# Performance work log

Measured on AMD Instinct MI355X. Metric: run time of the kernel, lower is better.

Reference implementation:

```python
import jax, jax.numpy as jnp
import numpy as np

N_A = 50000
N_B = 50000
E = 500000
D = 128


def setup_inputs() -> dict:
    key = jax.random.key(0)
    ks = jax.random.split(key, 16)
    s = 0.02
    inp = {
        "x_a": jax.random.normal(ks[0], (N_A, D), jnp.float32),
        "x_b": jax.random.normal(ks[1], (N_B, D), jnp.float32),
        # shared GraphEdgeWeight params
        "Wp": jax.random.normal(ks[2], (D, D), jnp.float32) * s,
        "bp": jnp.zeros((D,), jnp.float32),
        "Wc": jax.random.normal(ks[3], (D, D), jnp.float32) * s,
        "bc": jnp.zeros((D,), jnp.float32),
        "W1": jax.random.normal(ks[4], (D, 3 * D), jnp.float32) * s,
        "b1": jnp.zeros((D,), jnp.float32),
        "W2": jax.random.normal(ks[5], (1, D), jnp.float32) * s,
        "b2": jnp.zeros((1,), jnp.float32),
        # GraphConv params for edge type A->B
        "Wrel_ab": jax.random.normal(ks[6], (D, D), jnp.float32) * s,
        "brel_ab": jnp.zeros((D,), jnp.float32),
        "Wroot_ab": jax.random.normal(ks[7], (D, D), jnp.float32) * s,
        "broot_ab": jnp.zeros((D,), jnp.float32),
        # GraphConv params for edge type B->A
        "Wrel_ba": jax.random.normal(ks[8], (D, D), jnp.float32) * s,
        "brel_ba": jnp.zeros((D,), jnp.float32),
        "Wroot_ba": jax.random.normal(ks[9], (D, D), jnp.float32) * s,
        "broot_ba": jnp.zeros((D,), jnp.float32),
        # edge indices: row0 = src node ids, row1 = dst node ids
        "ei_ab": jax.random.randint(ks[10], (2, E), 0, N_A),
        "ei_ba": jax.random.randint(ks[11], (2, E), 0, N_B),
    }
    return inp


def _edge_type_conv(x_src, x_dst, ei, Wp, bp, Wc, bc, W1, b1, W2, b2,
                    Wrel, brel, Wroot, broot, n_dst):
    # gather endpoint features per edge  [E, D]
    par = x_src[ei[0]]
    cld = x_dst[ei[1]]
    # GraphEdgeWeight: encoders (Linear + LeakyReLU; dropout inactive in eval)
    ep = jax.nn.leaky_relu(par @ Wp.T + bp, negative_slope=0.01)
    ec = jax.nn.leaky_relu(cld @ Wc.T + bc, negative_slope=0.01)
    feat = jnp.concatenate([ep, ec, jnp.abs(par - cld)], axis=-1)  # [E, 3D]
    h = jax.nn.relu(feat @ W1.T + b1)                              # [E, D]
    w = jax.nn.sigmoid(h @ W2.T + b2)[:, 0]                        # [E]
    # GraphConv: out_i = Wrel @ sum_{j->i} w_e x_j + Wroot @ x_i (+ biases)
    msg = jax.ops.segment_sum(par * w[:, None], ei[1], num_segments=n_dst)
    return msg @ Wrel.T + brel + x_dst @ Wroot.T + broot


def reference(x_a, x_b, Wp, bp, Wc, bc, W1, b1, W2, b2,
              Wrel_ab, brel_ab, Wroot_ab, broot_ab,
              Wrel_ba, brel_ba, Wroot_ba, broot_ba,
              ei_ab, ei_ba):
    out_b = _edge_type_conv(x_a, x_b, ei_ab, Wp, bp, Wc, bc, W1, b1, W2, b2,
                            Wrel_ab, brel_ab, Wroot_ab, broot_ab, N_B)
    out_a = _edge_type_conv(x_b, x_a, ei_ba, Wp, bp, Wc, bc, W1, b1, W2, b2,
                            Wrel_ba, brel_ba, Wroot_ba, broot_ba, N_A)
    return out_a, out_b
```

## Files before the change

kernel.cpp:

```cpp
#include <hip/hip_runtime.h>
#include <hip/hip_bf16.h>

typedef unsigned short u16;
typedef __attribute__((ext_vector_type(8))) short bf16x8;
typedef __attribute__((ext_vector_type(2))) short s16x2;
typedef __attribute__((ext_vector_type(4))) float f32x4;

#define N_NODES 50000
#define EDGES 500000
#define WPT 31250
#define NWAVES 3125
#define NBLK 782

__device__ __forceinline__ u16 f2bf(float f) {
  return __builtin_bit_cast(u16, __float2bfloat16(f));
}
__device__ __forceinline__ float bf2f(u16 u) {
  return __builtin_bit_cast(float, ((unsigned)u) << 16);
}
__device__ __forceinline__ float bfe(bf16x8 v, int j) {
  return bf2f((u16)v[j]);
}

__device__ __forceinline__ void pk_atomic_bf16(u16* addr, float lo, float hi) {
#if __has_builtin(__builtin_amdgcn_global_atomic_fadd_v2bf16)
  s16x2 v;
  v[0] = (short)f2bf(lo);
  v[1] = (short)f2bf(hi);
  __builtin_amdgcn_global_atomic_fadd_v2bf16(
      (__attribute__((address_space(1))) s16x2*)addr, v);
#else
  unsigned* p = (unsigned*)addr;
  unsigned old = *p, assumed;
  do {
    assumed = old;
    float l2 = bf2f((u16)(assumed & 0xffff)) + lo;
    float h2 = bf2f((u16)(assumed >> 16)) + hi;
    unsigned nv = (unsigned)f2bf(l2) | ((unsigned)f2bf(h2) << 16);
    old = atomicCAS(p, assumed, nv);
  } while (old != assumed);
#endif
}

__global__ __launch_bounds__(256) void prep_weights(
    const float* __restrict__ Wp, const float* __restrict__ Wc,
    const float* __restrict__ W1,
    const float* __restrict__ Wrel_ab, const float* __restrict__ Wroot_ab,
    const float* __restrict__ Wrel_ba, const float* __restrict__ Wroot_ba,
    u16* __restrict__ out)
{
  int tid = blockIdx.x * 256 + threadIdx.x;
  int m = tid >> 14;
  int idx = tid & 16383;
  int r = idx >> 7;
  int c = idx & 127;
  float val;
  switch (m) {
    case 0: val = Wp[r * 128 + c]; break;
    case 1: val = Wc[r * 128 + c]; break;
    case 2: val = W1[r * 384 + c]; break;
    case 3: val = W1[r * 384 + 128 + c]; break;
    case 4: val = W1[r * 384 + 256 + c]; break;
    case 5: val = Wrel_ab[r * 128 + c]; break;
    case 6: val = Wroot_ab[r * 128 + c]; break;
    case 7: val = Wrel_ba[r * 128 + c]; break;
    default: val = Wroot_ba[r * 128 + c]; break;
  }
  out[tid] = f2bf(val);
}

__global__ __launch_bounds__(256) void cast_x(
    const float* __restrict__ xa, const float* __restrict__ xb,
    u16* __restrict__ oa, u16* __restrict__ ob)
{
  int t = blockIdx.x * 256 + threadIdx.x;
  const int HALF = (N_NODES * 128) / 8;
  const float* src;
  u16* dst;
  int idx;
  if (t < HALF) { src = xa; dst = oa; idx = t * 8; }
  else          { src = xb; dst = ob; idx = (t - HALF) * 8; }
  f32x4 a = *(const f32x4*)(src + idx);
  f32x4 b = *(const f32x4*)(src + idx + 4);
  bf16x8 o;
#pragma unroll
  for (int j = 0; j < 4; j++) {
    o[j]     = (short)f2bf(a[j]);
    o[j + 4] = (short)f2bf(b[j]);
  }
  *(bf16x8*)(dst + idx) = o;
}

__global__ __launch_bounds__(256) void encoder2(
    const u16* __restrict__ xa_bf, const u16* __restrict__ xb_bf,
    const u16* __restrict__ Wp_b, const float* __restrict__ bp,
    const u16* __restrict__ Wc_b, const float* __restrict__ bc,
    const u16* __restrict__ W1a_b, const float* __restrict__ b1,
    const u16* __restrict__ W1b_b,
    u16* __restrict__ u_a, u16* __restrict__ v_a,
    u16* __restrict__ u_b, u16* __restrict__ v_b)
{
  __shared__ u16 tile[4][2176];
  int widx = threadIdx.x >> 6;
  int w = blockIdx.x * 4 + widx;
  int type = (w >= NBLK * 4) ? 1 : 0;
  int nw = w - type * NBLK * 4;
  if (nw >= NWAVES) nw = NWAVES - 1;
  const u16* xbf = type ? xb_bf : xa_bf;
  u16* u_out = type ? u_b : u_a;
  u16* v_out = type ? v_b : v_a;
  int row0 = nw * 16;
  int lane = threadIdx.x & 63;
  int col = lane & 15;
  int quad = lane >> 4;
  u16* tl = tile[widx];

  bf16x8 af[4];
#pragma unroll
  for (int ks = 0; ks < 4; ks++)
    af[ks] = *(const bf16x8*)(xbf + (size_t)(row0 + col) * 128 + ks * 32 + quad * 8);

  f32x4 zero = {0.f, 0.f, 0.f, 0.f};

  for (int chain = 0; chain < 2; chain++) {
    const u16* Wenc = chain ? Wc_b : Wp_b;
    const float* benc = chain ? bc : bp;
    const u16* Wmix = chain ? W1b_b : W1a_b;
    const float* bmix = chain ? nullptr : b1;
    u16* outp = chain ? v_out : u_out;

    f32x4 acc[8];
#pragma unroll
    for (int nt = 0; nt < 8; nt++) acc[nt] = zero;
#pragma unroll
    for (int ks = 0; ks < 4; ks++) {
      const u16* wp = Wenc + col * 128 + ks * 32 + quad * 8;
#pragma unroll
      for (int nt = 0; nt < 8; nt++) {
        bf16x8 bf = *(const bf16x8*)(wp + nt * 2048);
        acc[nt] = __builtin_amdgcn_mfma_f32_16x16x32_bf16(af[ks], bf, acc[nt], 0, 0, 0);
      }
    }
#pragma unroll
    for (int nt = 0; nt < 8; nt++) {
      float be = benc[nt * 16 + col];
#pragma unroll
      for (int r = 0; r < 4; r++) {
        float v = acc[nt][r] + be;
        v = v > 0.f ? v : 0.01f * v;
        tl[(quad * 4 + r) * 136 + nt * 16 + col] = f2bf(v);
      }
    }
    bf16x8 a2[4];
#pragma unroll
    for (int ks = 0; ks < 4; ks++)
      a2[ks] = *(const bf16x8*)&tl[col * 136 + ks * 32 + quad * 8];

    f32x4 acc2[8];
#pragma unroll
    for (int nt = 0; nt < 8; nt++) acc2[nt] = zero;
#pragma unroll
    for (int ks = 0; ks < 4; ks++) {
      const u16* wp = Wmix + col * 128 + ks * 32 + quad * 8;
#pragma unroll
      for (int nt = 0; nt < 8; nt++) {
        bf16x8 bf = *(const bf16x8*)(wp + nt * 2048);
        acc2[nt] = __builtin_amdgcn_mfma_f32_16x16x32_bf16(a2[ks], bf, acc2[nt], 0, 0, 0);
      }
    }
#pragma unroll
    for (int nt = 0; nt < 8; nt++) {
      float bm = bmix ? bmix[nt * 16 + col] : 0.f;
#pragma unroll
      for (int r = 0; r < 4; r++)
        outp[(size_t)(row0 + quad * 4 + r) * 128 + nt * 16 + col] = f2bf(acc2[nt][r] + bm);
    }
  }
}

__global__ __launch_bounds__(256) void out_gemm2(
    const u16* __restrict__ xa_bf, const u16* __restrict__ xb_bf,
    const u16* __restrict__ msgX_a, const u16* __restrict__ msgX_b,
    const u16* __restrict__ Wrelba_b, const u16* __restrict__ Wrelab_b,
    const u16* __restrict__ Wrootba_b, const u16* __restrict__ Wrootab_b,
    const float* __restrict__ brel_ba, const float* __restrict__ broot_ba,
    const float* __restrict__ brel_ab, const float* __restrict__ broot_ab,
    float* __restrict__ out_a, float* __restrict__ out_b)
{
  int w = blockIdx.x * 4 + (threadIdx.x >> 6);
  int type = (w >= NBLK * 4) ? 1 : 0;
  int nw = w - type * NBLK * 4;
  if (nw >= NWAVES) return;
  const u16* xbf = type ? xb_bf : xa_bf;
  const u16* msg = type ? msgX_b : msgX_a;
  const u16* Wrel = type ? Wrelab_b : Wrelba_b;
  const u16* Wroot = type ? Wrootab_b : Wrootba_b;
  const float* brel = type ? brel_ab : brel_ba;
  const float* broot = type ? broot_ab : broot_ba;
  float* outp = type ? out_b : out_a;
  int row0 = nw * 16;
  int lane = threadIdx.x & 63;
  int col = lane & 15;
  int quad = lane >> 4;

  bf16x8 ax[4], am[4];
#pragma unroll
  for (int ks = 0; ks < 4; ks++) {
    ax[ks] = *(const bf16x8*)(xbf + (size_t)(row0 + col) * 128 + ks * 32 + quad * 8);
    am[ks] = *(const bf16x8*)(msg + (size_t)(row0 + col) * 128 + ks * 32 + quad * 8);
  }

  f32x4 zero = {0.f, 0.f, 0.f, 0.f};
  f32x4 acc[8];
#pragma unroll
  for (int nt = 0; nt < 8; nt++) acc[nt] = zero;
#pragma unroll
  for (int ks = 0; ks < 4; ks++) {
    const u16* wp1 = Wrel + col * 128 + ks * 32 + quad * 8;
    const u16* wp2 = Wroot + col * 128 + ks * 32 + quad * 8;
#pragma unroll
    for (int nt = 0; nt < 8; nt++) {
      bf16x8 b1f = *(const bf16x8*)(wp1 + nt * 2048);
      acc[nt] = __builtin_amdgcn_mfma_f32_16x16x32_bf16(am[ks], b1f, acc[nt], 0, 0, 0);
      bf16x8 b2f = *(const bf16x8*)(wp2 + nt * 2048);
      acc[nt] = __builtin_amdgcn_mfma_f32_16x16x32_bf16(ax[ks], b2f, acc[nt], 0, 0, 0);
    }
  }
#pragma unroll
  for (int nt = 0; nt < 8; nt++) {
    int c = nt * 16 + col;
    float b = brel[c] + broot[c];
#pragma unroll
    for (int r = 0; r < 4; r++)
      outp[(size_t)(row0 + quad * 4 + r) * 128 + c] = acc[nt][r] + b;
  }
}

__global__ __launch_bounds__(256) void edge_fused(
    const u16* __restrict__ xa_bf, const u16* __restrict__ xb_bf,
    const int* __restrict__ ei_ab, const int* __restrict__ ei_ba,
    const u16* __restrict__ W1c,
    const u16* __restrict__ u_a, const u16* __restrict__ v_a,
    const u16* __restrict__ u_b, const u16* __restrict__ v_b,
    const float* __restrict__ W2, const float* __restrict__ b2p,
    u16* __restrict__ msgX_a, u16* __restrict__ msgX_b)
{
  __shared__ u16 tld[4][2176];
  int widx = threadIdx.x >> 6;
  int w = blockIdx.x * 4 + widx;
  int type = (w >= WPT) ? 1 : 0;
  int e0 = (w - type * WPT) * 16;
  const u16* xs = type ? xb_bf : xa_bf;
  const u16* xd = type ? xa_bf : xb_bf;
  const int* ei = type ? ei_ba : ei_ab;
  const u16* uT = type ? u_b : u_a;
  const u16* vT = type ? v_a : v_b;
  u16* msgX     = type ? msgX_a : msgX_b;

  int lane = threadIdx.x & 63;
  int col = lane & 15;
  int quad = lane >> 4;

  int em = e0 + col;
  int si = ei[em];
  int di = ei[EDGES + em];

  bf16x8 af[4];
  bf16x8 df[4];
#pragma unroll
  for (int ks = 0; ks < 4; ks++) {
    af[ks] = *(const bf16x8*)(xs + (size_t)si * 128 + ks * 32 + quad * 8);
    bf16x8 d8 = *(const bf16x8*)(xd + (size_t)di * 128 + ks * 32 + quad * 8);
#pragma unroll
    for (int j = 0; j < 8; j++)
      df[ks][j] = (short)f2bf(__builtin_fabsf(bfe(af[ks], j) - bfe(d8, j)));
  }

  f32x4 zero = {0.f, 0.f, 0.f, 0.f};
  f32x4 acc[8];
#pragma unroll
  for (int nt = 0; nt < 8; nt++) acc[nt] = zero;
#pragma unroll
  for (int ks = 0; ks < 4; ks++) {
    const u16* wp = W1c + col * 128 + ks * 32 + quad * 8;
#pragma unroll
    for (int nt = 0; nt < 8; nt++) {
      bf16x8 bf = *(const bf16x8*)(wp + nt * 2048);
      acc[nt] = __builtin_amdgcn_mfma_f32_16x16x32_bf16(df[ks], bf, acc[nt], 0, 0, 0);
    }
  }

  u16* tl = tld[widx];
#pragma unroll
  for (int nt = 0; nt < 8; nt++)
#pragma unroll
    for (int r = 0; r < 4; r++)
      tl[(quad * 4 + r) * 136 + nt * 16 + col] = f2bf(acc[nt][r]);

  int e = e0 + (lane >> 2);
  int s2 = ei[e];
  int d2 = ei[EDGES + e];
  int c0 = (lane & 3) * 32;
  const u16* trow = &tl[(lane >> 2) * 136 + c0];
  const u16* urow = uT + (size_t)s2 * 128 + c0;
  const u16* vrow = vT + (size_t)d2 * 128 + c0;

  float p = 0.f;
#pragma unroll
  for (int k = 0; k < 4; k++) {
    bf16x8 tt = *(const bf16x8*)(trow + k * 8);
    bf16x8 uu = *(const bf16x8*)(urow + k * 8);
    bf16x8 vv = *(const bf16x8*)(vrow + k * 8);
    f32x4 w0 = *(const f32x4*)(W2 + c0 + k * 8);
    f32x4 w1 = *(const f32x4*)(W2 + c0 + k * 8 + 4);
#pragma unroll
    for (int j = 0; j < 4; j++) {
      float q0 = bfe(tt, j) + bfe(uu, j) + bfe(vv, j);
      if (q0 > 0.f) p += q0 * w0[j];
      float q1 = bfe(tt, j + 4) + bfe(uu, j + 4) + bfe(vv, j + 4);
      if (q1 > 0.f) p += q1 * w1[j];
    }
  }
  p += __shfl_xor(p, 1, 64);
  p += __shfl_xor(p, 2, 64);
  float wgt = 1.f / (1.f + __expf(-(p + b2p[0])));

#pragma unroll
  for (int ks = 0; ks < 4; ks++)
    *(bf16x8*)&tl[col * 136 + ks * 32 + quad * 8] = af[ks];

#pragma unroll
  for (int r = 0; r < 4; r++) {
    int src_lane = (quad * 4 + r) * 4;
    float wr = __shfl(wgt, src_lane, 64);
    int dr = __shfl(d2, src_lane, 64);
    u16* mrow = msgX + (size_t)dr * 128;
    const u16* xrow = &tl[(quad * 4 + r) * 136];
#pragma unroll
    for (int nt = 0; nt < 4; nt++) {
      int c = nt * 32 + col * 2;
      unsigned xv = *(const unsigned*)(xrow + c);
      pk_atomic_bf16(mrow + c, wr * bf2f((u16)(xv & 0xffff)),
                               wr * bf2f((u16)(xv >> 16)));
    }
  }
}

extern "C" void kernel_launch(void* const* d_in, const int* in_sizes, int n_in,
                              void* d_out, int out_size, void* d_ws, size_t ws_size,
                              hipStream_t stream) {
  const float* x_a      = (const float*)d_in[0];
  const float* x_b      = (const float*)d_in[1];
  const float* Wp       = (const float*)d_in[2];
  const float* bp       = (const float*)d_in[3];
  const float* Wc       = (const float*)d_in[4];
  const float* bc       = (const float*)d_in[5];
  const float* W1       = (const float*)d_in[6];
  const float* b1       = (const float*)d_in[7];
  const float* W2       = (const float*)d_in[8];
  const float* b2       = (const float*)d_in[9];
  const float* Wrel_ab  = (const float*)d_in[10];
  const float* brel_ab  = (const float*)d_in[11];
  const float* Wroot_ab = (const float*)d_in[12];
  const float* broot_ab = (const float*)d_in[13];
  const float* Wrel_ba  = (const float*)d_in[14];
  const float* brel_ba  = (const float*)d_in[15];
  const float* Wroot_ba = (const float*)d_in[16];
  const float* broot_ba = (const float*)d_in[17];
  const int*   ei_ab    = (const int*)d_in[18];
  const int*   ei_ba    = (const int*)d_in[19];

  char* ws = (char*)d_ws;
  u16* Wb        = (u16*)ws;
  u16* Wp_b      = Wb + 0 * 16384;
  u16* Wc_b      = Wb + 1 * 16384;
  u16* W1a_b     = Wb + 2 * 16384;
  u16* W1b_b     = Wb + 3 * 16384;
  u16* W1c_b     = Wb + 4 * 16384;
  u16* Wrelab_b  = Wb + 5 * 16384;
  u16* Wrootab_b = Wb + 6 * 16384;
  u16* Wrelba_b  = Wb + 7 * 16384;
  u16* Wrootba_b = Wb + 8 * 16384;

  u16* xa_bf   = (u16*)(ws + 1048576);
  u16* xb_bf   = (u16*)(ws + 13848576);
  u16* u_a     = (u16*)(ws + 26648576);
  u16* v_a     = (u16*)(ws + 39448576);
  u16* u_b     = (u16*)(ws + 52248576);
  u16* v_b     = (u16*)(ws + 65048576);
  u16* msgX_a  = (u16*)(ws + 77848576);
  u16* msgX_b  = (u16*)(ws + 90648576);

  float* out_a = (float*)d_out;
  float* out_b = out_a + (size_t)N_NODES * 128;

  hipMemsetAsync(msgX_a, 0, (size_t)2 * N_NODES * 128 * sizeof(u16), stream);

  prep_weights<<<576, 256, 0, stream>>>(Wp, Wc, W1, Wrel_ab, Wroot_ab,
                                        Wrel_ba, Wroot_ba, Wb);
  cast_x<<<6250, 256, 0, stream>>>(x_a, x_b, xa_bf, xb_bf);

  encoder2<<<2 * NBLK, 256, 0, stream>>>(xa_bf, xb_bf, Wp_b, bp, Wc_b, bc,
                                         W1a_b, b1, W1b_b, u_a, v_a, u_b, v_b);

  edge_fused<<<15625, 256, 0, stream>>>(xa_bf, xb_bf, ei_ab, ei_ba, W1c_b,
                                        u_a, v_a, u_b, v_b,
                                        W2, b2, msgX_a, msgX_b);

  out_gemm2<<<2 * NBLK, 256, 0, stream>>>(xa_bf, xb_bf, msgX_a, msgX_b,
                                          Wrelba_b, Wrelab_b,
                                          Wrootba_b, Wrootab_b,
                                          brel_ba, broot_ba, brel_ab, broot_ab,
                                          out_a, out_b);
}
```

Measured before the change: 698.6 us.

## Sort edges by destination and fuse edge processing with output GEMM

Builds a CSR-style ordering of edges by destination node: a histogram inside the cast kernel, a single-block prefix scan per edge type, and an atomic scatter sort. A new fused kernel lets each wave own 16 destination nodes. It walks their edges, computes edge weights, accumulates messages in fp32 shared memory instead of bf16 global atomics, then applies the Wrel/Wroot output GEMM directly. This removes the message buffer memset, the global packed-bf16 atomics and a separate output kernel. In exchange it adds sort kernels and a serial scan, and per-wave load imbalance from uneven degree, since each wave loops over a variable number of edges.

```diff
diff --git a/kernel.cpp b/kernel.cpp
--- a/kernel.cpp
+++ b/kernel.cpp
@@ -3,12 +3,10 @@
 
 typedef unsigned short u16;
 typedef __attribute__((ext_vector_type(8))) short bf16x8;
-typedef __attribute__((ext_vector_type(2))) short s16x2;
 typedef __attribute__((ext_vector_type(4))) float f32x4;
 
 #define N_NODES 50000
 #define EDGES 500000
-#define WPT 31250
 #define NWAVES 3125
 #define NBLK 782
 
@@ -20,26 +18,6 @@
 }
 __device__ __forceinline__ float bfe(bf16x8 v, int j) {
   return bf2f((u16)v[j]);
-}
-
-__device__ __forceinline__ void pk_atomic_bf16(u16* addr, float lo, float hi) {
-#if __has_builtin(__builtin_amdgcn_global_atomic_fadd_v2bf16)
-  s16x2 v;
-  v[0] = (short)f2bf(lo);
-  v[1] = (short)f2bf(hi);
-  __builtin_amdgcn_global_atomic_fadd_v2bf16(
-      (__attribute__((address_space(1))) s16x2*)addr, v);
-#else
-  unsigned* p = (unsigned*)addr;
-  unsigned old = *p, assumed;
-  do {
-    assumed = old;
-    float l2 = bf2f((u16)(assumed & 0xffff)) + lo;
-    float h2 = bf2f((u16)(assumed >> 16)) + hi;
-    unsigned nv = (unsigned)f2bf(l2) | ((unsigned)f2bf(h2) << 16);
-    old = atomicCAS(p, assumed, nv);
-  } while (old != assumed);
-#endif
 }
 
 __global__ __launch_bounds__(256) void prep_weights(
@@ -69,9 +47,11 @@
   out[tid] = f2bf(val);
 }
 
-__global__ __launch_bounds__(256) void cast_x(
+__global__ __launch_bounds__(256) void cast_x_hist(
     const float* __restrict__ xa, const float* __restrict__ xb,
-    u16* __restrict__ oa, u16* __restrict__ ob)
+    u16* __restrict__ oa, u16* __restrict__ ob,
+    const int* __restrict__ ei_ab, const int* __restrict__ ei_ba,
+    int* __restrict__ cnt)
 {
   int t = blockIdx.x * 256 + threadIdx.x;
   const int HALF = (N_NODES * 128) / 8;
@@ -89,6 +69,53 @@
     o[j + 4] = (short)f2bf(b[j]);
   }
   *(bf16x8*)(dst + idx) = o;
+
+  if (t < EDGES) {
+    atomicAdd(&cnt[ei_ab[EDGES + t]], 1);
+    atomicAdd(&cnt[N_NODES + ei_ba[EDGES + t]], 1);
+  }
+}
+
+__global__ __launch_bounds__(1024) void scan50k(
+    const int* __restrict__ cnt, int* __restrict__ cursor)
+{
+  __shared__ int part[1024];
+  const int* c = cnt + blockIdx.x * N_NODES;
+  int* cur = cursor + blockIdx.x * N_NODES;
+  int t = threadIdx.x;
+  int lo = t * 49;
+  int hi = lo + 49; if (hi > N_NODES) hi = N_NODES;
+  if (lo > N_NODES) lo = N_NODES;
+  int s = 0;
+  for (int i = lo; i < hi; i++) s += c[i];
+  part[t] = s;
+  __syncthreads();
+  for (int off = 1; off < 1024; off <<= 1) {
+    int v = (t >= off) ? part[t - off] : 0;
+    __syncthreads();
+    part[t] += v;
+    __syncthreads();
+  }
+  int base = (t == 0) ? 0 : part[t - 1];
+  for (int i = lo; i < hi; i++) { cur[i] = base; base += c[i]; }
+}
+
+__global__ __launch_bounds__(256) void edge_sort(
+    const int* __restrict__ ei_ab, const int* __restrict__ ei_ba,
+    int* __restrict__ cursor,
+    int2* __restrict__ sorted_ab, int2* __restrict__ sorted_ba)
+{
+  int t = blockIdx.x * 256 + threadIdx.x;
+  if (t < EDGES) {
+    int s = ei_ab[t], d = ei_ab[EDGES + t];
+    int pos = atomicAdd(&cursor[d], 1);
+    sorted_ab[pos] = make_int2(s, d);
+  } else if (t < 2 * EDGES) {
+    int tt = t - EDGES;
+    int s = ei_ba[tt], d = ei_ba[EDGES + tt];
+    int pos = atomicAdd(&cursor[N_NODES + d], 1);
+    sorted_ba[pos] = make_int2(s, d);
+  }
 }
 
 __global__ __launch_bounds__(256) void encoder2(
@@ -178,171 +205,177 @@
   }
 }
 
-__global__ __launch_bounds__(256) void out_gemm2(
+__global__ __launch_bounds__(256) void edge_mega(
     const u16* __restrict__ xa_bf, const u16* __restrict__ xb_bf,
-    const u16* __restrict__ msgX_a, const u16* __restrict__ msgX_b,
-    const u16* __restrict__ Wrelba_b, const u16* __restrict__ Wrelab_b,
-    const u16* __restrict__ Wrootba_b, const u16* __restrict__ Wrootab_b,
-    const float* __restrict__ brel_ba, const float* __restrict__ broot_ba,
-    const float* __restrict__ brel_ab, const float* __restrict__ broot_ab,
-    float* __restrict__ out_a, float* __restrict__ out_b)
-{
-  int w = blockIdx.x * 4 + (threadIdx.x >> 6);
-  int type = (w >= NBLK * 4) ? 1 : 0;
-  int nw = w - type * NBLK * 4;
-  if (nw >= NWAVES) return;
-  const u16* xbf = type ? xb_bf : xa_bf;
-  const u16* msg = type ? msgX_b : msgX_a;
-  const u16* Wrel = type ? Wrelab_b : Wrelba_b;
-  const u16* Wroot = type ? Wrootab_b : Wrootba_b;
-  const float* brel = type ? brel_ab : brel_ba;
-  const float* broot = type ? broot_ab : broot_ba;
-  float* outp = type ? out_b : out_a;
-  int row0 = nw * 16;
-  int lane = threadIdx.x & 63;
-  int col = lane & 15;
-  int quad = lane >> 4;
-
-  bf16x8 ax[4], am[4];
-#pragma unroll
-  for (int ks = 0; ks < 4; ks++) {
-    ax[ks] = *(const bf16x8*)(xbf + (size_t)(row0 + col) * 128 + ks * 32 + quad * 8);
-    am[ks] = *(const bf16x8*)(msg + (size_t)(row0 + col) * 128 + ks * 32 + quad * 8);
-  }
-
-  f32x4 zero = {0.f, 0.f, 0.f, 0.f};
-  f32x4 acc[8];
-#pragma unroll
-  for (int nt = 0; nt < 8; nt++) acc[nt] = zero;
-#pragma unroll
-  for (int ks = 0; ks < 4; ks++) {
-    const u16* wp1 = Wrel + col * 128 + ks * 32 + quad * 8;
-    const u16* wp2 = Wroot + col * 128 + ks * 32 + quad * 8;
-#pragma unroll
-    for (int nt = 0; nt < 8; nt++) {
-      bf16x8 b1f = *(const bf16x8*)(wp1 + nt * 2048);
-      acc[nt] = __builtin_amdgcn_mfma_f32_16x16x32_bf16(am[ks], b1f, acc[nt], 0, 0, 0);
-      bf16x8 b2f = *(const bf16x8*)(wp2 + nt * 2048);
-      acc[nt] = __builtin_amdgcn_mfma_f32_16x16x32_bf16(ax[ks], b2f, acc[nt], 0, 0, 0);
-    }
-  }
-#pragma unroll
-  for (int nt = 0; nt < 8; nt++) {
-    int c = nt * 16 + col;
-    float b = brel[c] + broot[c];
-#pragma unroll
-    for (int r = 0; r < 4; r++)
-      outp[(size_t)(row0 + quad * 4 + r) * 128 + c] = acc[nt][r] + b;
-  }
-}
-
-__global__ __launch_bounds__(256) void edge_fused(
-    const u16* __restrict__ xa_bf, const u16* __restrict__ xb_bf,
-    const int* __restrict__ ei_ab, const int* __restrict__ ei_ba,
+    const int2* __restrict__ sorted_ab, const int2* __restrict__ sorted_ba,
+    const int* __restrict__ cursor,
     const u16* __restrict__ W1c,
     const u16* __restrict__ u_a, const u16* __restrict__ v_a,
     const u16* __restrict__ u_b, const u16* __restrict__ v_b,
     const float* __restrict__ W2, const float* __restrict__ b2p,
-    u16* __restrict__ msgX_a, u16* __restrict__ msgX_b)
-{
-  __shared__ u16 tld[4][2176];
+    const u16* __restrict__ Wrelab, const u16* __restrict__ Wrootab,
+    const float* __restrict__ brel_ab, const float* __restrict__ broot_ab,
+    const u16* __restrict__ Wrelba, const u16* __restrict__ Wrootba,
+    const float* __restrict__ brel_ba, const float* __restrict__ broot_ba,
+    float* __restrict__ out_a, float* __restrict__ out_b)
+{
+  __shared__ u16 tls[4][2176];
+  __shared__ float msga[4][2112];
   int widx = threadIdx.x >> 6;
   int w = blockIdx.x * 4 + widx;
-  int type = (w >= WPT) ? 1 : 0;
-  int e0 = (w - type * WPT) * 16;
+  if (w >= 2 * NWAVES) w = 2 * NWAVES - 1;
+  int type = (w >= NWAVES) ? 1 : 0;
+  int g = w - type * NWAVES;
+  int n0 = g * 16;
+
   const u16* xs = type ? xb_bf : xa_bf;
   const u16* xd = type ? xa_bf : xb_bf;
-  const int* ei = type ? ei_ba : ei_ab;
+  const int2* se = type ? sorted_ba : sorted_ab;
+  const int* cur = cursor + type * N_NODES;
   const u16* uT = type ? u_b : u_a;
   const u16* vT = type ? v_a : v_b;
-  u16* msgX     = type ? msgX_a : msgX_b;
+  const u16* Wrel  = type ? Wrelba : Wrelab;
+  const u16* Wroot = type ? Wrootba : Wrootab;
+  const float* brel  = type ? brel_ba : brel_ab;
+  const float* broot = type ? broot_ba : broot_ab;
+  float* outp = type ? out_a : out_b;
+
+  int start = (n0 == 0) ? 0 : cur[n0 - 1];
+  int end = cur[n0 + 15];
 
   int lane = threadIdx.x & 63;
   int col = lane & 15;
   int quad = lane >> 4;
-
-  int em = e0 + col;
-  int si = ei[em];
-  int di = ei[EDGES + em];
-
-  bf16x8 af[4];
-  bf16x8 df[4];
+  u16* tl = tls[widx];
+  float* macc = msga[widx];
+
+  for (int i = lane; i < 2112; i += 64) macc[i] = 0.f;
+
+  bf16x8 ax[4];
+#pragma unroll
+  for (int ks = 0; ks < 4; ks++)
+    ax[ks] = *(const bf16x8*)(xd + (size_t)(n0 + col) * 128 + ks * 32 + quad * 8);
+
+  float b2 = b2p[0];
+  f32x4 zero = {0.f, 0.f, 0.f, 0.f};
+
+  for (int base = start; base < end; base += 16) {
+    int em = base + col;
+    if (em >= end) em = end - 1;
+    int2 pe = se[em];
+
+    bf16x8 af[4], df[4];
+#pragma unroll
+    for (int ks = 0; ks < 4; ks++) {
+      af[ks] = *(const bf16x8*)(xs + (size_t)pe.x * 128 + ks * 32 + quad * 8);
+      bf16x8 d8 = *(const bf16x8*)(xd + (size_t)pe.y * 128 + ks * 32 + quad * 8);
+#pragma unroll
+      for (int j = 0; j < 8; j++)
+        df[ks][j] = (short)f2bf(__builtin_fabsf(bfe(af[ks], j) - bfe(d8, j)));
+    }
+
+    f32x4 acc[8];
+#pragma unroll
+    for (int nt = 0; nt < 8; nt++) acc[nt] = zero;
+#pragma unroll
+    for (int ks = 0; ks < 4; ks++) {
+      const u16* wp = W1c + col * 128 + ks * 32 + quad * 8;
+#pragma unroll
+      for (int nt = 0; nt < 8; nt++) {
+        bf16x8 bf = *(const bf16x8*)(wp + nt * 2048);
+        acc[nt] = __builtin_amdgcn_mfma_f32_16x16x32_bf16(df[ks], bf, acc[nt], 0, 0, 0);
+      }
+    }
+#pragma unroll
+    for (int nt = 0; nt < 8; nt++)
+#pragma unroll
+      for (int r = 0; r < 4; r++)
+        tl[(quad * 4 + r) * 136 + nt * 16 + col] = f2bf(acc[nt][r]);
+
+    int e2 = base + (lane >> 2);
+    bool evalid = e2 < end;
+    int2 q = se[evalid ? e2 : end - 1];
+    int c0 = (lane & 3) * 32;
+    const u16* trow = &tl[(lane >> 2) * 136 + c0];
+    const u16* urow = uT + (size_t)q.x * 128 + c0;
+    const u16* vrow = vT + (size_t)q.y * 128 + c0;
+
+    float p = 0.f;
+#pragma unroll
+    for (int k = 0; k < 4; k++) {
+      bf16x8 tt = *(const bf16x8*)(trow + k * 8);
+      bf16x8 uu = *(const bf16x8*)(urow + k * 8);
+      bf16x8 vv = *(const bf16x8*)(vrow + k * 8);
+      f32x4 w0 = *(const f32x4*)(W2 + c0 + k * 8);
+      f32x4 w1 = *(const f32x4*)(W2 + c0 + k * 8 + 4);
+#pragma unroll
+      for (int j = 0; j < 4; j++) {
+        float q0 = bfe(tt, j) + bfe(uu, j) + bfe(vv, j);
+        if (q0 > 0.f) p += q0 * w0[j];
+        float q1 = bfe(tt, j + 4) + bfe(uu, j + 4) + bfe(vv, j + 4);
+        if (q1 > 0.f) p += q1 * w1[j];
+      }
+    }
+    p += __shfl_xor(p, 1, 64);
+    p += __shfl_xor(p, 2, 64);
+    float wgt = evalid ? 1.f / (1.f + __expf(-(p + b2))) : 0.f;
+    int dloc = q.y - n0;
+
+#pragma unroll
+    for (int ks = 0; ks < 4; ks++)
+      *(bf16x8*)&tl[col * 136 + ks * 32 + quad * 8] = af[ks];
+
+#pragma unroll
+    for (int r = 0; r < 4; r++) {
+      int src_lane = (quad * 4 + r) * 4;
+      float wr = __shfl(wgt, src_lane, 64);
+      int ldr = __shfl(dloc, src_lane, 64);
+      const u16* xrow = &tl[(quad * 4 + r) * 136];
+      float* mrow = &macc[ldr * 132];
+#pragma unroll
+      for (int nt = 0; nt < 4; nt++) {
+        int c = nt * 32 + col * 2;
+        unsigned xv = *(const unsigned*)(xrow + c);
+        atomicAdd(&mrow[c],     wr * bf2f((u16)(xv & 0xffff)));
+        atomicAdd(&mrow[c + 1], wr * bf2f((u16)(xv >> 16)));
+      }
+    }
+  }
+
+  bf16x8 am[4];
 #pragma unroll
   for (int ks = 0; ks < 4; ks++) {
-    af[ks] = *(const bf16x8*)(xs + (size_t)si * 128 + ks * 32 + quad * 8);
-    bf16x8 d8 = *(const bf16x8*)(xd + (size_t)di * 128 + ks * 32 + quad * 8);
-#pragma unroll
-    for (int j = 0; j < 8; j++)
-      df[ks][j] = (short)f2bf(__builtin_fabsf(bfe(af[ks], j) - bfe(d8, j)));
-  }
-
-  f32x4 zero = {0.f, 0.f, 0.f, 0.f};
-  f32x4 acc[8];
-#pragma unroll
-  for (int nt = 0; nt < 8; nt++) acc[nt] = zero;
+    f32x4 a0 = *(const f32x4*)&macc[col * 132 + ks * 32 + quad * 8];
+    f32x4 a1 = *(const f32x4*)&macc[col * 132 + ks * 32 + quad * 8 + 4];
+#pragma unroll
+    for (int j = 0; j < 4; j++) {
+      am[ks][j]     = (short)f2bf(a0[j]);
+      am[ks][j + 4] = (short)f2bf(a1[j]);
+    }
+  }
+
+  f32x4 acc2[8];
+#pragma unroll
+  for (int nt = 0; nt < 8; nt++) acc2[nt] = zero;
 #pragma unroll
   for (int ks = 0; ks < 4; ks++) {
-    const u16* wp = W1c + col * 128 + ks * 32 + quad * 8;
+    const u16* wp1 = Wrel + col * 128 + ks * 32 + quad * 8;
+    const u16* wp2 = Wroot + col * 128 + ks * 32 + quad * 8;
 #pragma unroll
     for (int nt = 0; nt < 8; nt++) {
-      bf16x8 bf = *(const bf16x8*)(wp + nt * 2048);
-      acc[nt] = __builtin_amdgcn_mfma_f32_16x16x32_bf16(df[ks], bf, acc[nt], 0, 0, 0);
-    }
-  }
-
-  u16* tl = tld[widx];
-#pragma unroll
-  for (int nt = 0; nt < 8; nt++)
+      bf16x8 b1f = *(const bf16x8*)(wp1 + nt * 2048);
+      acc2[nt] = __builtin_amdgcn_mfma_f32_16x16x32_bf16(am[ks], b1f, acc2[nt], 0, 0, 0);
+      bf16x8 b2f = *(const bf16x8*)(wp2 + nt * 2048);
+      acc2[nt] = __builtin_amdgcn_mfma_f32_16x16x32_bf16(ax[ks], b2f, acc2[nt], 0, 0, 0);
+    }
+  }
+#pragma unroll
+  for (int nt = 0; nt < 8; nt++) {
+    int c = nt * 16 + col;
+    float b = brel[c] + broot[c];
 #pragma unroll
     for (int r = 0; r < 4; r++)
-      tl[(quad * 4 + r) * 136 + nt * 16 + col] = f2bf(acc[nt][r]);
-
-  int e = e0 + (lane >> 2);
-  int s2 = ei[e];
-  int d2 = ei[EDGES + e];
-  int c0 = (lane & 3) * 32;
-  const u16* trow = &tl[(lane >> 2) * 136 + c0];
-  const u16* urow = uT + (size_t)s2 * 128 + c0;
-  const u16* vrow = vT + (size_t)d2 * 128 + c0;
-
-  float p = 0.f;
-#pragma unroll
-  for (int k = 0; k < 4; k++) {
-    bf16x8 tt = *(const bf16x8*)(trow + k * 8);
-    bf16x8 uu = *(const bf16x8*)(urow + k * 8);
-    bf16x8 vv = *(const bf16x8*)(vrow + k * 8);
-    f32x4 w0 = *(const f32x4*)(W2 + c0 + k * 8);
-    f32x4 w1 = *(const f32x4*)(W2 + c0 + k * 8 + 4);
-#pragma unroll
-    for (int j = 0; j < 4; j++) {
-      float q0 = bfe(tt, j) + bfe(uu, j) + bfe(vv, j);
-      if (q0 > 0.f) p += q0 * w0[j];
-      float q1 = bfe(tt, j + 4) + bfe(uu, j + 4) + bfe(vv, j + 4);
-      if (q1 > 0.f) p += q1 * w1[j];
-    }
-  }
-  p += __shfl_xor(p, 1, 64);
-  p += __shfl_xor(p, 2, 64);
-  float wgt = 1.f / (1.f + __expf(-(p + b2p[0])));
-
-#pragma unroll
-  for (int ks = 0; ks < 4; ks++)
-    *(bf16x8*)&tl[col * 136 + ks * 32 + quad * 8] = af[ks];
-
-#pragma unroll
-  for (int r = 0; r < 4; r++) {
-    int src_lane = (quad * 4 + r) * 4;
-    float wr = __shfl(wgt, src_lane, 64);
-    int dr = __shfl(d2, src_lane, 64);
-    u16* mrow = msgX + (size_t)dr * 128;
-    const u16* xrow = &tl[(quad * 4 + r) * 136];
-#pragma unroll
-    for (int nt = 0; nt < 4; nt++) {
-      int c = nt * 32 + col * 2;
-      unsigned xv = *(const unsigned*)(xrow + c);
-      pk_atomic_bf16(mrow + c, wr * bf2f((u16)(xv & 0xffff)),
-                               wr * bf2f((u16)(xv >> 16)));
-    }
+      outp[(size_t)(n0 + quad * 4 + r) * 128 + c] = acc2[nt][r] + b;
   }
 }
 
@@ -388,28 +421,28 @@
   u16* v_a     = (u16*)(ws + 39448576);
   u16* u_b     = (u16*)(ws + 52248576);
   u16* v_b     = (u16*)(ws + 65048576);
-  u16* msgX_a  = (u16*)(ws + 77848576);
-  u16* msgX_b  = (u16*)(ws + 90648576);
+  int* cnt     = (int*)(ws + 77848576);
+  int* cursor  = (int*)(ws + 78248576);
+  int2* sorted_ab = (int2*)(ws + 78648576);
+  int2* sorted_ba = (int2*)(ws + 82648576);
 
   float* out_a = (float*)d_out;
   float* out_b = out_a + (size_t)N_NODES * 128;
 
-  hipMemsetAsync(msgX_a, 0, (size_t)2 * N_NODES * 128 * sizeof(u16), stream);
+  hipMemsetAsync(cnt, 0, 2 * N_NODES * sizeof(int), stream);
 
   prep_weights<<<576, 256, 0, stream>>>(Wp, Wc, W1, Wrel_ab, Wroot_ab,
                                         Wrel_ba, Wroot_ba, Wb);
-  cast_x<<<6250, 256, 0, stream>>>(x_a, x_b, xa_bf, xb_bf);
+  cast_x_hist<<<6250, 256, 0, stream>>>(x_a, x_b, xa_bf, xb_bf, ei_ab, ei_ba, cnt);
+  scan50k<<<2, 1024, 0, stream>>>(cnt, cursor);
+  edge_sort<<<3907, 256, 0, stream>>>(ei_ab, ei_ba, cursor, sorted_ab, sorted_ba);
 
   encoder2<<<2 * NBLK, 256, 0, stream>>>(xa_bf, xb_bf, Wp_b, bp, Wc_b, bc,
                                          W1a_b, b1, W1b_b, u_a, v_a, u_b, v_b);
 
-  edge_fused<<<15625, 256, 0, stream>>>(xa_bf, xb_bf, ei_ab, ei_ba, W1c_b,
-                                        u_a, v_a, u_b, v_b,
-                                        W2, b2, msgX_a, msgX_b);
-
-  out_gemm2<<<2 * NBLK, 256, 0, stream>>>(xa_bf, xb_bf, msgX_a, msgX_b,
-                                          Wrelba_b, Wrelab_b,
-                                          Wrootba_b, Wrootab_b,
-                                          brel_ba, broot_ba, brel_ab, broot_ab,
-                                          out_a, out_b);
-}
+  edge_mega<<<1563, 256, 0, stream>>>(xa_bf, xb_bf, sorted_ab, sorted_ba, cursor,
+                                      W1c_b, u_a, v_a, u_b, v_b, W2, b2,
+                                      Wrelab_b, Wrootab_b, brel_ab, broot_ab,
+                                      Wrelba_b, Wrootba_b, brel_ba, broot_ba,
+                                      out_a, out_b);
+}
```

After: 1.363 ms. 95.1% more time.
